# Kernel optimization log

Measured on AMD Instinct MI355X. Metric: run time of the kernel, lower is better.

Reference implementation:

```python
import jax, jax.numpy as jnp
import numpy as np

EPS = 1e-6      # delta in ixaxaar/pytorch-dnc util.py and Memory.reset
CLIP = 20.0     # DNC default controller-output clip
M, Wc, R, H, IN, OUT = 10, 20, 1, 256, 27, 128
NN_IN = IN + R * Wc                 # 47 controller input size
IFACE = R * Wc + 3 * Wc + 5 * R + 3  # 88 interface vector size


def _cosine_weights(mem, keys, strengths):
    # mem (B,M,Wc), keys (B,K,Wc), strengths (B,K) -> softmax over cells of scaled cosine sim
    mem_n = mem / (jnp.linalg.norm(mem, axis=2, keepdims=True) + EPS)
    key_n = keys / (jnp.linalg.norm(keys, axis=2, keepdims=True) + EPS)
    d = jnp.einsum('bkw,bmw->bkm', key_n, mem_n)
    return jax.nn.softmax(d * strengths[:, :, None], axis=2)


def _dnc_classifier(x, W_ih, W_hh, b_ih, b_hh, W_xi, b_xi, W_fc, b_fc):
    B, T, _ = x.shape
    # ixaxaar's dnc.py builds inputs[t] = cat(x_t, last_read) ONCE with the initial
    # (zero) last_read, so read vectors never feed the next-step input.
    pad = jnp.zeros((B, R * Wc), x.dtype)
    eye_mask = 1.0 - jnp.eye(M, dtype=x.dtype)

    def step(state, x_t):
        h, c, mem, link, prec, rw, ww, usage = state
        # ---- LSTM controller (1 hidden layer, torch gate order i,f,g,o) ----
        inp = jnp.concatenate([x_t, pad], axis=1)                 # (B,47)
        gates = inp @ W_ih.T + b_ih + h @ W_hh.T + b_hh           # (B,4H)
        i, f, g, o = jnp.split(gates, 4, axis=1)
        c = jax.nn.sigmoid(f) * c + jax.nn.sigmoid(i) * jnp.tanh(g)
        h = jax.nn.sigmoid(o) * jnp.tanh(c)
        out = jnp.clip(h, -CLIP, CLIP)
        # ---- interface vector ----
        xi = out @ W_xi.T + b_xi                                  # (B,88)
        p = R * Wc
        rk = jnp.tanh(xi[:, :p]).reshape(B, R, Wc)                # read keys
        rs = jax.nn.softplus(xi[:, p:p + R]); p += R              # read strengths
        wk = jnp.tanh(xi[:, p:p + Wc]).reshape(B, 1, Wc); p += Wc # write key
        ws = jax.nn.softplus(xi[:, p:p + 1]); p += 1              # write strength
        ev = jax.nn.sigmoid(xi[:, p:p + Wc]); p += Wc             # erase vector
        wv = jnp.tanh(xi[:, p:p + Wc]); p += Wc                   # write vector
        fg = jax.nn.sigmoid(xi[:, p:p + R]); p += R               # free gates
        ag = jax.nn.sigmoid(xi[:, p:p + 1]); p += 1               # allocation gate
        wg = jax.nn.sigmoid(xi[:, p:p + 1]); p += 1               # write gate
        rm = jax.nn.softmax(xi[:, p:p + 3 * R].reshape(B, R, 3), axis=-1)  # read modes (b,f,c)
        # ---- usage (uses PREVIOUS write/read weights) ----
        usage = usage + (1 - usage) * ww
        usage = usage * jnp.prod(1 - fg[:, :, None] * rw, axis=1)
        # ---- write weighting: content + allocation (sort-based free list) ----
        cw = _cosine_weights(mem, wk, ws)[:, 0]                   # (B,M)
        u2 = EPS + (1 - EPS) * usage
        phi = jnp.argsort(u2, axis=1)
        su = jnp.take_along_axis(u2, phi, axis=1)
        prod_excl = jnp.cumprod(jnp.concatenate([jnp.ones((B, 1), u2.dtype), su], axis=1), axis=1)[:, :-1]
        alloc = jnp.take_along_axis((1 - su) * prod_excl, jnp.argsort(phi, axis=1), axis=1)
        ww = wg * (ag * alloc + (1 - ag) * cw)                    # (B,M)
        # ---- erase + write memory ----
        mem = mem * (1 - ww[:, :, None] * ev[:, None, :]) + ww[:, :, None] * wv[:, None, :]
        # ---- temporal link matrix + precedence ----
        link = (1 - ww[:, :, None] - ww[:, None, :]) * link + ww[:, :, None] * prec[:, None, :]
        link = link * eye_mask
        prec = (1 - jnp.sum(ww, axis=1, keepdims=True)) * prec + ww
        # ---- read weighting (content + forward/backward temporal) ----
        cwr = _cosine_weights(mem, rk, rs)                        # (B,R,M)
        fw = jnp.einsum('brm,bnm->brn', rw, link)                 # forward  = L @ w
        bw = jnp.einsum('brm,bmn->brn', rw, link)                 # backward = L^T @ w
        rw = rm[:, :, 0:1] * bw + rm[:, :, 1:2] * fw + rm[:, :, 2:3] * cwr
        return (h, c, mem, link, prec, rw, ww, usage), None

    z = jnp.zeros
    state0 = (z((B, H), x.dtype), z((B, H), x.dtype),
              jnp.full((B, M, Wc), EPS, x.dtype), z((B, M, M), x.dtype),
              z((B, M), x.dtype), jnp.full((B, R, M), EPS, x.dtype),
              jnp.full((B, M), EPS, x.dtype), z((B, M), x.dtype))
    (h, *_), _ = jax.lax.scan(step, state0, jnp.swapaxes(x, 0, 1))
    # classifier head: fc1 on final controller hidden state
    return h @ W_fc.T + b_fc


def setup_inputs() -> dict:
    key = jax.random.key(0)
    ks = jax.random.split(key, 10)
    B, T = 128, 512
    kb = 1.0 / np.sqrt(H)
    u = lambda kk, shape: jax.random.uniform(kk, shape, jnp.float32, -kb, kb)
    return {
        'x': jax.random.normal(ks[0], (B, T, IN), jnp.float32),
        'input_lengths': jax.random.randint(ks[1], (B,), 1, T + 1).astype(jnp.int32),
        'W_ih': u(ks[2], (4 * H, NN_IN)),
        'W_hh': u(ks[3], (4 * H, H)),
        'b_ih': u(ks[4], (4 * H,)),
        'b_hh': u(ks[5], (4 * H,)),
        'W_xi': u(ks[6], (IFACE, H)),
        'b_xi': u(ks[7], (IFACE,)),
        'W_fc': u(ks[8], (OUT, H)),
        'b_fc': u(ks[9], (OUT,)),
    }


def reference(x, input_lengths, W_ih, W_hh, b_ih, b_hh, W_xi, b_xi, W_fc, b_fc):
    # input_lengths is unpacked and discarded by DNCClassifier.forward
    return _dnc_classifier(x, W_ih, W_hh, b_ih, b_hh, W_xi, b_xi, W_fc, b_fc)
```

## Files before the change

kernel.cpp:

```cpp
#include <hip/hip_runtime.h>
#include <hip/hip_fp16.h>


typedef _Float16 h2t __attribute__((ext_vector_type(2)));
typedef unsigned int u32x4 __attribute__((ext_vector_type(4)));

#if defined(__has_builtin)
#  if __has_builtin(__builtin_amdgcn_fdot2)
#    define HAVE_FDOT2 1
#  endif
#endif

__device__ __forceinline__ h2t bc2(unsigned int v) {
  union { unsigned int u; h2t h; } x; x.u = v; return x.h;
}
__device__ __forceinline__ unsigned int pk(float a, float b) {
  union { h2t h; unsigned int u; } x;
  x.h[0] = (_Float16)a; x.h[1] = (_Float16)b;
  return x.u;
}
__device__ __forceinline__ float fdot2f(h2t a, h2t b, float c) {
#ifdef HAVE_FDOT2
  return __builtin_amdgcn_fdot2(a, b, c, false);
#else
  return c + (float)a[0] * (float)b[0] + (float)a[1] * (float)b[1];
#endif
}
__device__ __forceinline__ float dot4(u32x4 w, u32x4 h, float a) {
  a = fdot2f(bc2(w[0]), bc2(h[0]), a);
  a = fdot2f(bc2(w[1]), bc2(h[1]), a);
  a = fdot2f(bc2(w[2]), bc2(h[2]), a);
  a = fdot2f(bc2(w[3]), bc2(h[3]), a);
  return a;
}
__device__ __forceinline__ float sigmf_(float x) {
  return 1.f / (1.f + __expf(-x));
}
__device__ __forceinline__ float tanhf_(float x) {
  float xc = fminf(15.f, fmaxf(-15.f, x));
  float e = __expf(2.f * xc);
  return (e - 1.f) / (e + 1.f);
}

#define WS_P_OFF      0ull
#define WS_WSCAN_OFF  134217728ull
#define WS_WLDS_OFF   134643712ull
#define WS_WSTR_OFF   134725632ull
#define WS_NEED       134742016ull

__global__ void prep_w(const float* __restrict__ W_hh,
                       unsigned char* __restrict__ ws) {
  int idx = blockIdx.x * 256 + threadIdx.x;
  unsigned int* dst; int j, f;
  if (idx < 106496) {
    j = idx; dst = (unsigned int*)(ws + WS_WSCAN_OFF); f = (j >> 2) >> 9;
  } else if (idx < 126976) {
    j = idx - 106496; dst = (unsigned int*)(ws + WS_WLDS_OFF);
    f = 52 + ((j >> 2) >> 9);
  } else {
    j = idx - 126976; dst = (unsigned int*)(ws + WS_WSTR_OFF);
    f = 62 + ((j >> 2) >> 9);
  }
  int e = j & 3, v = (j >> 2) & 511;
  int q = f >> 2, g = f & 3;
  int k2 = ((v >> 8) << 6) + 4 * q + e;
  int r = g * 256 + (v & 255);
  dst[j] = pk(W_hh[r * 256 + 2 * k2], W_hh[r * 256 + 2 * k2 + 1]);
}

__global__ __launch_bounds__(256) void prep_p(const float* __restrict__ x,
                                              const float* __restrict__ W_ih,
                                              const float* __restrict__ b_ih,
                                              const float* __restrict__ b_hh,
                                              unsigned char* __restrict__ ws) {
  __shared__ unsigned int sX[64][14];
  const int u = threadIdx.x;
  const int t = blockIdx.x >> 1;
  const int b0 = (blockIdx.x & 1) << 6;
  unsigned int wih[4][14];
  float bias[4];
#pragma unroll
  for (int g = 0; g < 4; ++g) {
    const float* row = W_ih + (size_t)(g * 256 + u) * 47;
    bias[g] = b_ih[g * 256 + u] + b_hh[g * 256 + u];
#pragma unroll
    for (int j = 0; j < 14; ++j) {
      float a = row[2 * j];
      float b = (2 * j + 1 < 27) ? row[2 * j + 1] : 0.f;
      wih[g][j] = pk(a, b);
    }
  }
#pragma unroll 1
  for (int j = u; j < 896; j += 256) {
    int row = j / 14, c2 = j - 14 * row;
    const float* xr = x + ((size_t)(b0 + row) * 512 + t) * 27;
    float a = xr[2 * c2];
    float bb = (2 * c2 + 1 < 27) ? xr[2 * c2 + 1] : 0.f;
    sX[row][c2] = pk(a, bb);
  }
  __syncthreads();
  uint2* Pout = (uint2*)(ws + WS_P_OFF);
#pragma unroll 2
  for (int p = 0; p < 64; ++p) {
    float a0 = bias[0], a1 = bias[1], a2 = bias[2], a3 = bias[3];
#pragma unroll
    for (int j = 0; j < 14; ++j) {
      h2t xx = bc2(sX[p][j]);
      a0 = fdot2f(bc2(wih[0][j]), xx, a0);
      a1 = fdot2f(bc2(wih[1][j]), xx, a1);
      a2 = fdot2f(bc2(wih[2][j]), xx, a2);
      a3 = fdot2f(bc2(wih[3][j]), xx, a3);
    }
    uint2 o; o.x = pk(a0, a1); o.y = pk(a2, a3);
    Pout[((size_t)t * 128 + (b0 + p)) * 256 + u] = o;
  }
}

__global__ __launch_bounds__(512, 2) void scan_k(
    const unsigned char* __restrict__ ws, const float* __restrict__ W_fc,
    const float* __restrict__ b_fc, float* __restrict__ out) {
  __shared__ u32x4 sWq[10 * 512];
  __shared__ u32x4 sHq[2][32];
  __shared__ float4 sAcc[256];
  __shared__ float sHF[256];
  const int v = threadIdx.x;
  const int b = blockIdx.x;
  const int half = v >> 8;
  const int u = v & 255;

  u32x4 wr[52];
  {
    const u32x4* wsc = (const u32x4*)(ws + WS_WSCAN_OFF);
#pragma unroll
    for (int f = 0; f < 52; ++f) wr[f] = wsc[f * 512 + v];
  }
  {
    const u32x4* wld = (const u32x4*)(ws + WS_WLDS_OFF);
#pragma unroll
    for (int fl = 0; fl < 10; ++fl) sWq[fl * 512 + v] = wld[fl * 512 + v];
  }
  const u32x4* wstr = (const u32x4*)(ws + WS_WSTR_OFF);

  if (v < 64) {
    u32x4 z = {0u, 0u, 0u, 0u};
    ((u32x4*)sHq)[v] = z;
  }
  const uint2* Pbuf = (const uint2*)(ws + WS_P_OFF);
  uint2 pP = make_uint2(0u, 0u);
  if (half == 0) pP = Pbuf[(size_t)b * 256 + u];
  float c = 0.f, hval = 0.f;
  __syncthreads();

#pragma unroll 1
  for (int t = 0; t < 512; ++t) {
    u32x4 tw0 = wstr[0 * 512 + v];
    u32x4 tw1 = wstr[1 * 512 + v];

    const u32x4* rd = &sHq[t & 1][half << 4];
    float acc0 = 0.f, acc1 = 0.f, acc2 = 0.f, acc3 = 0.f;
#pragma unroll
    for (int q = 0; q < 13; ++q) {
      u32x4 hq = rd[q];
      acc0 = dot4(wr[q * 4 + 0], hq, acc0);
      acc1 = dot4(wr[q * 4 + 1], hq, acc1);
      acc2 = dot4(wr[q * 4 + 2], hq, acc2);
      acc3 = dot4(wr[q * 4 + 3], hq, acc3);
    }
    {
      u32x4 hq = rd[13];
      acc0 = dot4(sWq[0 * 512 + v], hq, acc0);
      acc1 = dot4(sWq[1 * 512 + v], hq, acc1);
      acc2 = dot4(sWq[2 * 512 + v], hq, acc2);
      acc3 = dot4(sWq[3 * 512 + v], hq, acc3);
    }
    {
      u32x4 hq = rd[14];
      acc0 = dot4(sWq[4 * 512 + v], hq, acc0);
      acc1 = dot4(sWq[5 * 512 + v], hq, acc1);
      acc2 = dot4(sWq[6 * 512 + v], hq, acc2);
      acc3 = dot4(sWq[7 * 512 + v], hq, acc3);
    }
    {
      u32x4 hq = rd[15];
      acc0 = dot4(sWq[8 * 512 + v], hq, acc0);
      acc1 = dot4(sWq[9 * 512 + v], hq, acc1);
      acc2 = dot4(tw0, hq, acc2);
      acc3 = dot4(tw1, hq, acc3);
    }

    uint2 pPn = pP;
    if (half) {
      sAcc[u] = make_float4(acc0, acc1, acc2, acc3);
    } else {
      int tn = (t < 511) ? (t + 1) : 511;
      pPn = Pbuf[((size_t)tn * 128 + b) * 256 + u];
    }
    __syncthreads();

    if (!half) {
      float4 oth = sAcc[u];
      h2t p01 = bc2(pP.x), p23 = bc2(pP.y);
      float gi = acc0 + oth.x + (float)p01[0];
      float gf = acc1 + oth.y + (float)p01[1];
      float gg = acc2 + oth.z + (float)p23[0];
      float go = acc3 + oth.w + (float)p23[1];
      c = sigmf_(gf) * c + sigmf_(gi) * tanhf_(gg);
      hval = sigmf_(go) * tanhf_(c);
      ((_Float16*)(&sHq[(t + 1) & 1][0]))[u] = (_Float16)hval;
    }
    pP = pPn;
    __syncthreads();
  }

  if (!half) sHF[u] = hval;
  __syncthreads();
  if (v < 128) {
    const float4* wrow = (const float4*)(W_fc + (size_t)v * 256);
    float a = b_fc[v];
#pragma unroll 8
    for (int q = 0; q < 64; ++q) {
      float4 w = wrow[q];
      float4 hh = ((const float4*)sHF)[q];
      a += w.x * hh.x + w.y * hh.y + w.z * hh.z + w.w * hh.w;
    }
    out[(size_t)b * 128 + v] = a;
  }
}

extern "C" void kernel_launch(void* const* d_in, const int* in_sizes, int n_in,
                              void* d_out, int out_size, void* d_ws,
                              size_t ws_size, hipStream_t stream) {
  const float* x    = (const float*)d_in[0];
  const float* W_ih = (const float*)d_in[2];
  const float* W_hh = (const float*)d_in[3];
  const float* b_ih = (const float*)d_in[4];
  const float* b_hh = (const float*)d_in[5];
  const float* W_fc = (const float*)d_in[8];
  const float* b_fc = (const float*)d_in[9];
  unsigned char* ws = (unsigned char*)d_ws;

  if (ws_size < WS_NEED) return;

  prep_w<<<512, 256, 0, stream>>>(W_hh, ws);
  prep_p<<<1024, 256, 0, stream>>>(x, W_ih, b_ih, b_hh, ws);
  scan_k<<<128, 512, 0, stream>>>(ws, W_fc, b_fc, (float*)d_out);
}
```

Measured before the change: 871.3 us.

## Split LSTM recurrent matvec across 1024 threads with 4-way K reduction and readlane broadcast

```diff
diff --git a/kernel.cpp b/kernel.cpp
--- a/kernel.cpp
+++ b/kernel.cpp
@@ -26,11 +26,12 @@
   return c + (float)a[0] * (float)b[0] + (float)a[1] * (float)b[1];
 #endif
 }
-__device__ __forceinline__ float dot4(u32x4 w, u32x4 h, float a) {
-  a = fdot2f(bc2(w[0]), bc2(h[0]), a);
-  a = fdot2f(bc2(w[1]), bc2(h[1]), a);
-  a = fdot2f(bc2(w[2]), bc2(h[2]), a);
-  a = fdot2f(bc2(w[3]), bc2(h[3]), a);
+__device__ __forceinline__ float dot4s(u32x4 w, unsigned h0, unsigned h1,
+                                       unsigned h2, unsigned h3, float a) {
+  a = fdot2f(bc2(w[0]), bc2(h0), a);
+  a = fdot2f(bc2(w[1]), bc2(h1), a);
+  a = fdot2f(bc2(w[2]), bc2(h2), a);
+  a = fdot2f(bc2(w[3]), bc2(h3), a);
   return a;
 }
 __device__ __forceinline__ float sigmf_(float x) {
@@ -42,30 +43,22 @@
   return (e - 1.f) / (e + 1.f);
 }
 
-#define WS_P_OFF      0ull
-#define WS_WSCAN_OFF  134217728ull
-#define WS_WLDS_OFF   134643712ull
-#define WS_WSTR_OFF   134725632ull
-#define WS_NEED       134742016ull
+#define WS_P_OFF 0ull
+#define WS_W_OFF 134217728ull
+#define WS_NEED  134742016ull
 
 __global__ void prep_w(const float* __restrict__ W_hh,
                        unsigned char* __restrict__ ws) {
   int idx = blockIdx.x * 256 + threadIdx.x;
-  unsigned int* dst; int j, f;
-  if (idx < 106496) {
-    j = idx; dst = (unsigned int*)(ws + WS_WSCAN_OFF); f = (j >> 2) >> 9;
-  } else if (idx < 126976) {
-    j = idx - 106496; dst = (unsigned int*)(ws + WS_WLDS_OFF);
-    f = 52 + ((j >> 2) >> 9);
-  } else {
-    j = idx - 126976; dst = (unsigned int*)(ws + WS_WSTR_OFF);
-    f = 62 + ((j >> 2) >> 9);
-  }
-  int e = j & 3, v = (j >> 2) & 511;
-  int q = f >> 2, g = f & 3;
-  int k2 = ((v >> 8) << 6) + 4 * q + e;
-  int r = g * 256 + (v & 255);
-  dst[j] = pk(W_hh[r * 256 + 2 * k2], W_hh[r * 256 + 2 * k2 + 1]);
+  int e = idx & 3; int qid = idx >> 2;
+  int v = qid & 1023; int f2 = qid >> 10;
+  int jh = f2 >> 2, g = f2 & 3;
+  int s = (v >> 6) & 3;
+  int u = ((v >> 8) << 6) + (v & 63);
+  int k2 = 32 * s + 4 * jh + e;
+  int r = g * 256 + u;
+  ((unsigned int*)(ws + WS_W_OFF))[idx] =
+      pk(W_hh[r * 256 + 2 * k2], W_hh[r * 256 + 2 * k2 + 1]);
 }
 
 __global__ __launch_bounds__(256) void prep_p(const float* __restrict__ x,
@@ -116,112 +109,97 @@
   }
 }
 
-__global__ __launch_bounds__(512, 2) void scan_k(
+#define JH(jh, W0, W1, W2, W3)                                               \
+  {                                                                          \
+    unsigned hh0 = (unsigned)__builtin_amdgcn_readlane((int)hrs, base + 4*jh + 0); \
+    unsigned hh1 = (unsigned)__builtin_amdgcn_readlane((int)hrs, base + 4*jh + 1); \
+    unsigned hh2 = (unsigned)__builtin_amdgcn_readlane((int)hrs, base + 4*jh + 2); \
+    unsigned hh3 = (unsigned)__builtin_amdgcn_readlane((int)hrs, base + 4*jh + 3); \
+    acc0 = dot4s(W0, hh0, hh1, hh2, hh3, acc0);                              \
+    acc1 = dot4s(W1, hh0, hh1, hh2, hh3, acc1);                              \
+    acc2 = dot4s(W2, hh0, hh1, hh2, hh3, acc2);                              \
+    acc3 = dot4s(W3, hh0, hh1, hh2, hh3, acc3);                              \
+  }
+
+__global__ __launch_bounds__(1024, 1) void scan_k(
     const unsigned char* __restrict__ ws, const float* __restrict__ W_fc,
     const float* __restrict__ b_fc, float* __restrict__ out) {
-  __shared__ u32x4 sWq[10 * 512];
-  __shared__ u32x4 sHq[2][32];
-  __shared__ float4 sAcc[256];
+  __shared__ u32x4 sW[5 * 1024];
+  __shared__ float4 sRed[2][4][256];
+  __shared__ unsigned int sHd[128];
   __shared__ float sHF[256];
-  const int v = threadIdx.x;
-  const int b = blockIdx.x;
-  const int half = v >> 8;
-  const int u = v & 255;
-
-  u32x4 wr[52];
-  {
-    const u32x4* wsc = (const u32x4*)(ws + WS_WSCAN_OFF);
-#pragma unroll
-    for (int f = 0; f < 52; ++f) wr[f] = wsc[f * 512 + v];
-  }
-  {
-    const u32x4* wld = (const u32x4*)(ws + WS_WLDS_OFF);
-#pragma unroll
-    for (int fl = 0; fl < 10; ++fl) sWq[fl * 512 + v] = wld[fl * 512 + v];
-  }
-  const u32x4* wstr = (const u32x4*)(ws + WS_WSTR_OFF);
-
-  if (v < 64) {
-    u32x4 z = {0u, 0u, 0u, 0u};
-    ((u32x4*)sHq)[v] = z;
-  }
+  const int v = threadIdx.x, b = blockIdx.x;
+  const int w = v >> 6, l = v & 63;
+  const int s = w & 3, ug = w >> 2;
+  const int u = (ug << 6) + l;
+  const bool upd = (s == ug);
+  const u32x4* Wq = (const u32x4*)(ws + WS_W_OFF);
+
+  u32x4 wr[20];
+#pragma unroll
+  for (int f = 0; f < 20; ++f) wr[f] = Wq[f * 1024 + v];
+#pragma unroll
+  for (int f = 0; f < 5; ++f) sW[f * 1024 + v] = Wq[(20 + f) * 1024 + v];
+  if (v < 128) sHd[v] = 0u;
+
   const uint2* Pbuf = (const uint2*)(ws + WS_P_OFF);
   uint2 pP = make_uint2(0u, 0u);
-  if (half == 0) pP = Pbuf[(size_t)b * 256 + u];
+  if (upd) pP = Pbuf[(size_t)b * 256 + u];
   float c = 0.f, hval = 0.f;
   __syncthreads();
+  unsigned hr0 = sHd[l], hr1 = sHd[64 + l];
+  const int base = (s & 1) << 5;
 
 #pragma unroll 1
   for (int t = 0; t < 512; ++t) {
-    u32x4 tw0 = wstr[0 * 512 + v];
-    u32x4 tw1 = wstr[1 * 512 + v];
-
-    const u32x4* rd = &sHq[t & 1][half << 4];
+    u32x4 twA0 = Wq[25 * 1024 + v];
+    u32x4 twA1 = Wq[26 * 1024 + v];
+    u32x4 twA2 = Wq[27 * 1024 + v];
+    unsigned hrs = (s < 2) ? hr0 : hr1;
     float acc0 = 0.f, acc1 = 0.f, acc2 = 0.f, acc3 = 0.f;
-#pragma unroll
-    for (int q = 0; q < 13; ++q) {
-      u32x4 hq = rd[q];
-      acc0 = dot4(wr[q * 4 + 0], hq, acc0);
-      acc1 = dot4(wr[q * 4 + 1], hq, acc1);
-      acc2 = dot4(wr[q * 4 + 2], hq, acc2);
-      acc3 = dot4(wr[q * 4 + 3], hq, acc3);
-    }
-    {
-      u32x4 hq = rd[13];
-      acc0 = dot4(sWq[0 * 512 + v], hq, acc0);
-      acc1 = dot4(sWq[1 * 512 + v], hq, acc1);
-      acc2 = dot4(sWq[2 * 512 + v], hq, acc2);
-      acc3 = dot4(sWq[3 * 512 + v], hq, acc3);
-    }
-    {
-      u32x4 hq = rd[14];
-      acc0 = dot4(sWq[4 * 512 + v], hq, acc0);
-      acc1 = dot4(sWq[5 * 512 + v], hq, acc1);
-      acc2 = dot4(sWq[6 * 512 + v], hq, acc2);
-      acc3 = dot4(sWq[7 * 512 + v], hq, acc3);
-    }
-    {
-      u32x4 hq = rd[15];
-      acc0 = dot4(sWq[8 * 512 + v], hq, acc0);
-      acc1 = dot4(sWq[9 * 512 + v], hq, acc1);
-      acc2 = dot4(tw0, hq, acc2);
-      acc3 = dot4(tw1, hq, acc3);
-    }
-
-    uint2 pPn = pP;
-    if (half) {
-      sAcc[u] = make_float4(acc0, acc1, acc2, acc3);
-    } else {
-      int tn = (t < 511) ? (t + 1) : 511;
-      pPn = Pbuf[((size_t)tn * 128 + b) * 256 + u];
-    }
+    JH(0, wr[0], wr[1], wr[2], wr[3]);
+    JH(1, wr[4], wr[5], wr[6], wr[7]);
+    JH(2, wr[8], wr[9], wr[10], wr[11]);
+    u32x4 twB0 = Wq[28 * 1024 + v];
+    u32x4 twB1 = Wq[29 * 1024 + v];
+    u32x4 twB2 = Wq[30 * 1024 + v];
+    u32x4 twB3 = Wq[31 * 1024 + v];
+    JH(3, wr[12], wr[13], wr[14], wr[15]);
+    JH(4, wr[16], wr[17], wr[18], wr[19]);
+    JH(5, sW[0 * 1024 + v], sW[1 * 1024 + v], sW[2 * 1024 + v], sW[3 * 1024 + v]);
+    JH(6, sW[4 * 1024 + v], twA0, twA1, twA2);
+    JH(7, twB0, twB1, twB2, twB3);
+
+    sRed[t & 1][s][u] = make_float4(acc0, acc1, acc2, acc3);
     __syncthreads();
 
-    if (!half) {
-      float4 oth = sAcc[u];
+    if (upd) {
+      float4 r0 = sRed[t & 1][0][u], r1 = sRed[t & 1][1][u];
+      float4 r2 = sRed[t & 1][2][u], r3 = sRed[t & 1][3][u];
       h2t p01 = bc2(pP.x), p23 = bc2(pP.y);
-      float gi = acc0 + oth.x + (float)p01[0];
-      float gf = acc1 + oth.y + (float)p01[1];
-      float gg = acc2 + oth.z + (float)p23[0];
-      float go = acc3 + oth.w + (float)p23[1];
+      float gi = r0.x + r1.x + r2.x + r3.x + (float)p01[0];
+      float gf = r0.y + r1.y + r2.y + r3.y + (float)p01[1];
+      float gg = r0.z + r1.z + r2.z + r3.z + (float)p23[0];
+      float go = r0.w + r1.w + r2.w + r3.w + (float)p23[1];
       c = sigmf_(gf) * c + sigmf_(gi) * tanhf_(gg);
       hval = sigmf_(go) * tanhf_(c);
-      ((_Float16*)(&sHq[(t + 1) & 1][0]))[u] = (_Float16)hval;
-    }
-    pP = pPn;
+      ((unsigned short*)sHd)[u] = (unsigned short)(pk(hval, 0.f) & 0xffffu);
+      if (t == 511) sHF[u] = hval;
+      int tn = (t < 511) ? t + 1 : 511;
+      pP = Pbuf[((size_t)tn * 128 + b) * 256 + u];
+    }
     __syncthreads();
-  }
-
-  if (!half) sHF[u] = hval;
-  __syncthreads();
+    hr0 = sHd[l]; hr1 = sHd[64 + l];
+  }
+
   if (v < 128) {
     const float4* wrow = (const float4*)(W_fc + (size_t)v * 256);
     float a = b_fc[v];
 #pragma unroll 8
     for (int q = 0; q < 64; ++q) {
-      float4 w = wrow[q];
+      float4 wv = wrow[q];
       float4 hh = ((const float4*)sHF)[q];
-      a += w.x * hh.x + w.y * hh.y + w.z * hh.z + w.w * hh.w;
+      a += wv.x * hh.x + wv.y * hh.y + wv.z * hh.z + wv.w * hh.w;
     }
     out[(size_t)b * 128 + v] = a;
   }
@@ -243,5 +221,5 @@
 
   prep_w<<<512, 256, 0, stream>>>(W_hh, ws);
   prep_p<<<1024, 256, 0, stream>>>(x, W_ih, b_ih, b_hh, ws);
-  scan_k<<<128, 512, 0, stream>>>(ws, W_fc, b_fc, (float*)d_out);
-}
+  scan_k<<<128, 1024, 0, stream>>>(ws, W_fc, b_fc, (float*)d_out);
+}
```

After: 1.637 ms. 1.88x slower.
